# Kernel tuning notes

Measured on AMD Instinct MI355X. Metric: run time of the kernel, lower is better.

The kernel has to match this reference:

```python
import jax, jax.numpy as jnp
import numpy as np

K = 16          # buckets per codeblock (2**treeDepth)
DEPTH = 4       # tree depth
C = 256         # codeblockCount
IN_FEATURES = 4096
OUT_FEATURES = 4096
N_ROWS = 4096

_BASE_TREE = np.array([
    [-1,-1,0,-1,0,0,0,-1,0,0,0,0,0,0,0],[-1,-1,0,-1,0,0,0,1,0,0,0,0,0,0,0],
    [-1,-1,0,1,0,0,0,0,-1,0,0,0,0,0,0],[-1,-1,0,1,0,0,0,0,1,0,0,0,0,0,0],
    [-1,1,0,0,-1,0,0,0,0,-1,0,0,0,0,0],[-1,1,0,0,-1,0,0,0,0,1,0,0,0,0,0],
    [-1,1,0,0,1,0,0,0,0,0,-1,0,0,0,0],[-1,1,0,0,1,0,0,0,0,0,1,0,0,0,0],
    [1,0,-1,0,0,-1,0,0,0,0,0,-1,0,0,0],[1,0,-1,0,0,-1,0,0,0,0,0,1,0,0,0],
    [1,0,-1,0,0,1,0,0,0,0,0,0,-1,0,0],[1,0,-1,0,0,1,0,0,0,0,0,0,1,0,0],
    [1,0,1,0,0,0,-1,0,0,0,0,0,0,-1,0],[1,0,1,0,0,0,-1,0,0,0,0,0,0,1,0],
    [1,0,1,0,0,0,1,0,0,0,0,0,0,0,-1],[1,0,1,0,0,0,1,0,0,0,0,0,0,0,1]],
    dtype=np.float32)

def _make_tree_des_matrix(c):
    # NOTE: original code initializes with ONES, then overwrites diagonal blocks
    m = np.ones((c * K, c * (K - 1)), dtype=np.float32)
    for i in range(c):
        m[i*K:(i+1)*K, i*(K-1):(i+1)*(K-1)] = _BASE_TREE
    return m

def _make_selection_matrix(c):
    base = np.zeros((K - 1, DEPTH), dtype=np.float32)
    base[0, 0] = 1.0
    for i in range(1, K - 1):
        base[i, int(np.log2(i + 1))] = 1.0
    m = np.zeros((c * (K - 1), c * DEPTH), dtype=np.float32)
    for i in range(c):
        m[i*(K-1):(i+1)*(K-1), i*DEPTH:(i+1)*DEPTH] = base
    return m

def setup_inputs() -> dict:
    key = jax.random.key(0)
    k1, k2, k3, k4 = jax.random.split(key, 4)
    inputMatrix = jax.random.normal(k1, (N_ROWS, IN_FEATURES), dtype=jnp.float32)
    dims = jax.random.randint(k2, (C * DEPTH,), 0, IN_FEATURES)
    selection_matrix = jnp.asarray(_make_selection_matrix(C))
    thresholds = jax.random.normal(k3, (C * (K - 1), 1), dtype=jnp.float32)
    tree_des_mat = jnp.asarray(_make_tree_des_matrix(C))
    lut = jax.random.normal(k4, (OUT_FEATURES, C, K), dtype=jnp.float32)
    return {"inputMatrix": inputMatrix, "dims": dims,
            "selection_matrix": selection_matrix, "thresholds": thresholds,
            "tree_des_mat": tree_des_mat, "lut": lut}

def reference(inputMatrix, dims, selection_matrix, thresholds, tree_des_mat, lut):
    n = inputMatrix.shape[0]
    c = lut.shape[1]
    # gather the tree-split feature dims: (N, C*DEPTH)
    chosen = inputMatrix[:, dims]
    # (C*15, N)
    subtracted = selection_matrix @ chosen.T - thresholds
    tanh_h = jnp.tanh(subtracted)
    sign_ste = jnp.sign(subtracted) - jax.lax.stop_gradient(tanh_h) + tanh_h
    # (C*16, N) -> (N, C, 16)
    tree_result = (tree_des_mat @ sign_ste).T.reshape(n, c, K)
    encoding_soft = jax.nn.softmax(tree_result, axis=2)
    index = jnp.argmax(encoding_soft, axis=2)
    encoding_hard = jax.nn.one_hot(index, K, dtype=encoding_soft.dtype)
    Encoded = encoding_hard - jax.lax.stop_gradient(encoding_soft) + encoding_soft
    # LUT lookup: einsum 'nij,kij->nki' + sum over i, fused to 'nij,kij->nk'
    out = jnp.einsum('nij,kij->nk', Encoded, lut)
    return out
```

## Files before the change

### kernel.cpp

```cpp
#include <hip/hip_runtime.h>

#define N_ROWS 4096
#define IN_F   4096
#define OUT_F  4096
#define C_CB   256
#define KDIM   4096

typedef short bf16x8 __attribute__((ext_vector_type(8)));
typedef float f32x4  __attribute__((ext_vector_type(4)));

union ABFrag { unsigned long long u[2]; bf16x8 v; };

__device__ __forceinline__ unsigned int f2bf(float f) {
    unsigned int u = __builtin_bit_cast(unsigned int, f);
    return (u + 0x7FFFu + ((u >> 16) & 1u)) >> 16;
}

__global__ void k_idx(const float* __restrict__ input, const int* __restrict__ dims,
                      const float* __restrict__ thr, unsigned char* __restrict__ idx4) {
    const int n = blockIdx.x;
    const int c = threadIdx.x;
    const float* row = input + (size_t)n * IN_F;
    int4 d = *(const int4*)(dims + c * 4);
    const float* th = thr + c * 15;
    float x0 = row[d.x], x1 = row[d.y], x2 = row[d.z], x3 = row[d.w];
    int b0 = x0 > th[0];
    int j1 = 1 + b0;
    int b1 = x1 > th[j1];
    int j2 = 2 * j1 + 1 + b1;
    int b2 = x2 > th[j2];
    int j3 = 2 * j2 + 1 + b2;
    int b3 = x3 > th[j3];
    int idx = (b0 << 3) | (b1 << 2) | (b2 << 1) | b3;
    int other = __shfl_xor(idx, 1);
    if (!(c & 1))
        idx4[(c >> 1) * N_ROWS + n] = (unsigned char)(idx | (other << 4));
}

__global__ void k_cvt(const float* __restrict__ lut, unsigned short* __restrict__ lutb) {
    const int i = (blockIdx.x * blockDim.x + threadIdx.x) * 8;
    float4 a = *(const float4*)(lut + i);
    float4 b = *(const float4*)(lut + i + 4);
    uint4 o;
    o.x = f2bf(a.x) | (f2bf(a.y) << 16);
    o.y = f2bf(a.z) | (f2bf(a.w) << 16);
    o.z = f2bf(b.x) | (f2bf(b.y) << 16);
    o.w = f2bf(b.z) | (f2bf(b.w) << 16);
    *(uint4*)(lutb + i) = o;
}

#define BM 128
#define BN 128
#define BKT 64

template<bool STAGE_FP32>
__global__ __launch_bounds__(256, 4) void k_gemm(const unsigned short* __restrict__ lutb,
                                                 const float* __restrict__ lutf,
                                                 const unsigned char* __restrict__ idx4,
                                                 float* __restrict__ out) {
    __shared__ unsigned char smem[16384 + BN * BKT * 2];
    unsigned char* ish = smem;
    unsigned char* bsh = smem + 16384;

    const int t   = threadIdx.x;
    const int l15 = t & 15;
    const int q   = (t >> 4) & 3;
    const int w   = t >> 6;
    const int wm  = w >> 1, wn = w & 1;
    const int m0  = blockIdx.y * BM;
    const int n0  = blockIdx.x * BN;

    #pragma unroll
    for (int qq = 0; qq < 4; qq++) {
        int L = qq * 256 + t;
        const unsigned char* g = idx4 + (size_t)(L >> 3) * N_ROWS + m0 + (L & 7) * 16;
        __builtin_amdgcn_global_load_lds(
            (const __attribute__((address_space(1))) void*)g,
            (__attribute__((address_space(3))) void*)(ish + L * 16), 16, 0, 0);
    }

    f32x4 acc[4][4];
    #pragma unroll
    for (int mi = 0; mi < 4; mi++)
        #pragma unroll
        for (int ni = 0; ni < 4; ni++)
            acc[mi][ni] = (f32x4){0.f, 0.f, 0.f, 0.f};

    const int xorv = l15 & 7;
    const int bRowByte = (wn * 64 + l15) * (BKT * 2);
    const int aByte = wm * 64 + l15 * 4;
    const int qh4  = (q >> 1) * 4;
    const unsigned int sub8 = (q & 1) << 3;

    for (int kb = 0; kb < KDIM; kb += BKT) {
        if (!STAGE_FP32) {
            #pragma unroll
            for (int qq = 0; qq < 4; qq++) {
                int L = qq * 256 + t;
                int r = L >> 3, p = L & 7;
                int c = p ^ (r & 7);
                const unsigned short* g = lutb + (size_t)(n0 + r) * KDIM + kb + c * 8;
                __builtin_amdgcn_global_load_lds(
                    (const __attribute__((address_space(1))) void*)g,
                    (__attribute__((address_space(3))) void*)(bsh + L * 16), 16, 0, 0);
            }
        } else {
            #pragma unroll
            for (int qq = 0; qq < 4; qq++) {
                int L = qq * 256 + t;
                int r = L >> 3, p = L & 7;
                int c = p ^ (r & 7);
                const float* g = lutf + (size_t)(n0 + r) * KDIM + kb + c * 8;
                float4 f0 = *(const float4*)g;
                float4 f1 = *(const float4*)(g + 4);
                uint4 o;
                o.x = f2bf(f0.x) | (f2bf(f0.y) << 16);
                o.y = f2bf(f0.z) | (f2bf(f0.w) << 16);
                o.z = f2bf(f1.x) | (f2bf(f1.y) << 16);
                o.w = f2bf(f1.z) | (f2bf(f1.w) << 16);
                *(uint4*)(bsh + L * 16) = o;
            }
        }
        __syncthreads();

        #pragma unroll
        for (int s = 0; s < 2; s++) {
            const int cbp = (kb >> 5) + s;

            ABFrag bf[4];
            const int chunkOff = ((s * 4 + q) ^ xorv) * 16;
            #pragma unroll
            for (int ni = 0; ni < 4; ni++)
                bf[ni].v = *(const bf16x8*)(bsh + bRowByte + ni * (16 * BKT * 2) + chunkOff);

            const unsigned int w32 = *(const unsigned int*)(ish + cbp * 128 + aByte);

            ABFrag af[4];
            #pragma unroll
            for (int mi = 0; mi < 4; mi++) {
                unsigned int T = (w32 >> (mi * 8 + qh4)) & 0xFu;
                unsigned int rel = T - sub8;
                unsigned long long sh = 0x3F80ull << ((rel & 3) << 4);
                af[mi].u[0] = (rel < 4u) ? sh : 0ull;
                af[mi].u[1] = ((rel - 4u) < 4u) ? sh : 0ull;
            }

            #pragma unroll
            for (int mi = 0; mi < 4; mi++)
                #pragma unroll
                for (int ni = 0; ni < 4; ni++)
                    acc[mi][ni] = __builtin_amdgcn_mfma_f32_16x16x32_bf16(
                        af[mi].v, bf[ni].v, acc[mi][ni], 0, 0, 0);
        }
        __syncthreads();
    }

    #pragma unroll
    for (int mi = 0; mi < 4; mi++) {
        #pragma unroll
        for (int ni = 0; ni < 4; ni++) {
            const int col = n0 + wn * 64 + ni * 16 + l15;
            #pragma unroll
            for (int r = 0; r < 4; r++) {
                const int row = m0 + wm * 64 + 4 * (q * 4 + r) + mi;
                out[(size_t)row * OUT_F + col] = acc[mi][ni][r];
            }
        }
    }
}

extern "C" void kernel_launch(void* const* d_in, const int* in_sizes, int n_in,
                              void* d_out, int out_size, void* d_ws, size_t ws_size,
                              hipStream_t stream) {
    const float* input = (const float*)d_in[0];
    const int*   dims  = (const int*)d_in[1];
    const float* thr   = (const float*)d_in[3];
    const float* lut   = (const float*)d_in[5];
    float* out = (float*)d_out;

    const size_t lutbBytes = (size_t)OUT_F * KDIM * 2;
    const size_t idxBytes  = (size_t)(C_CB / 2) * N_ROWS;

    dim3 gg(OUT_F / BN, N_ROWS / BM);

    if (ws_size >= lutbBytes + idxBytes) {
        unsigned short* lutb = (unsigned short*)d_ws;
        unsigned char*  idx4 = (unsigned char*)d_ws + lutbBytes;
        k_idx<<<N_ROWS, C_CB, 0, stream>>>(input, dims, thr, idx4);
        k_cvt<<<(OUT_F * KDIM) / (256 * 8), 256, 0, stream>>>(lut, lutb);
        k_gemm<false><<<gg, 256, 0, stream>>>(lutb, lut, idx4, out);
    } else {
        unsigned char* idx4 = (unsigned char*)d_ws;
        k_idx<<<N_ROWS, C_CB, 0, stream>>>(input, dims, thr, idx4);
        k_gemm<true><<<gg, 256, 0, stream>>>(nullptr, lut, idx4, out);
    }
}
```

Baseline: 314.5 us.

## Load GEMM operands directly from global memory and fuse prep kernels

```diff
diff --git a/kernel.cpp b/kernel.cpp
--- a/kernel.cpp
+++ b/kernel.cpp
@@ -16,8 +16,42 @@
     return (u + 0x7FFFu + ((u >> 16) & 1u)) >> 16;
 }
 
-__global__ void k_idx(const float* __restrict__ input, const int* __restrict__ dims,
-                      const float* __restrict__ thr, unsigned char* __restrict__ idx4) {
+__global__ void k_prep(const float* __restrict__ input, const int* __restrict__ dims,
+                       const float* __restrict__ thr, unsigned char* __restrict__ idx4,
+                       const float* __restrict__ lut, unsigned short* __restrict__ lutb) {
+    if (blockIdx.x < N_ROWS) {
+        const int n = blockIdx.x;
+        const int c = threadIdx.x;
+        const float* row = input + (size_t)n * IN_F;
+        int4 d = *(const int4*)(dims + c * 4);
+        const float* th = thr + c * 15;
+        float x0 = row[d.x], x1 = row[d.y], x2 = row[d.z], x3 = row[d.w];
+        int b0 = x0 > th[0];
+        int j1 = 1 + b0;
+        int b1 = x1 > th[j1];
+        int j2 = 2 * j1 + 1 + b1;
+        int b2 = x2 > th[j2];
+        int j3 = 2 * j2 + 1 + b2;
+        int b3 = x3 > th[j3];
+        int idx = (b0 << 3) | (b1 << 2) | (b2 << 1) | b3;
+        int other = __shfl_xor(idx, 1);
+        if (!(c & 1))
+            idx4[(c >> 1) * N_ROWS + n] = (unsigned char)(idx | (other << 4));
+    } else {
+        const int i = ((blockIdx.x - N_ROWS) * 256 + threadIdx.x) * 8;
+        float4 a = *(const float4*)(lut + i);
+        float4 b = *(const float4*)(lut + i + 4);
+        uint4 o;
+        o.x = f2bf(a.x) | (f2bf(a.y) << 16);
+        o.y = f2bf(a.z) | (f2bf(a.w) << 16);
+        o.z = f2bf(b.x) | (f2bf(b.y) << 16);
+        o.w = f2bf(b.z) | (f2bf(b.w) << 16);
+        *(uint4*)(lutb + i) = o;
+    }
+}
+
+__global__ void k_idx_only(const float* __restrict__ input, const int* __restrict__ dims,
+                           const float* __restrict__ thr, unsigned char* __restrict__ idx4) {
     const int n = blockIdx.x;
     const int c = threadIdx.x;
     const float* row = input + (size_t)n * IN_F;
@@ -37,31 +71,14 @@
         idx4[(c >> 1) * N_ROWS + n] = (unsigned char)(idx | (other << 4));
 }
 
-__global__ void k_cvt(const float* __restrict__ lut, unsigned short* __restrict__ lutb) {
-    const int i = (blockIdx.x * blockDim.x + threadIdx.x) * 8;
-    float4 a = *(const float4*)(lut + i);
-    float4 b = *(const float4*)(lut + i + 4);
-    uint4 o;
-    o.x = f2bf(a.x) | (f2bf(a.y) << 16);
-    o.y = f2bf(a.z) | (f2bf(a.w) << 16);
-    o.z = f2bf(b.x) | (f2bf(b.y) << 16);
-    o.w = f2bf(b.z) | (f2bf(b.w) << 16);
-    *(uint4*)(lutb + i) = o;
-}
-
 #define BM 128
 #define BN 128
-#define BKT 64
 
-template<bool STAGE_FP32>
+template<bool B_IS_BF16>
 __global__ __launch_bounds__(256, 4) void k_gemm(const unsigned short* __restrict__ lutb,
                                                  const float* __restrict__ lutf,
                                                  const unsigned char* __restrict__ idx4,
                                                  float* __restrict__ out) {
-    __shared__ unsigned char smem[16384 + BN * BKT * 2];
-    unsigned char* ish = smem;
-    unsigned char* bsh = smem + 16384;
-
     const int t   = threadIdx.x;
     const int l15 = t & 15;
     const int q   = (t >> 4) & 3;
@@ -70,15 +87,6 @@
     const int m0  = blockIdx.y * BM;
     const int n0  = blockIdx.x * BN;
 
-    #pragma unroll
-    for (int qq = 0; qq < 4; qq++) {
-        int L = qq * 256 + t;
-        const unsigned char* g = idx4 + (size_t)(L >> 3) * N_ROWS + m0 + (L & 7) * 16;
-        __builtin_amdgcn_global_load_lds(
-            (const __attribute__((address_space(1))) void*)g,
-            (__attribute__((address_space(3))) void*)(ish + L * 16), 16, 0, 0);
-    }
-
     f32x4 acc[4][4];
     #pragma unroll
     for (int mi = 0; mi < 4; mi++)
@@ -86,73 +94,61 @@
         for (int ni = 0; ni < 4; ni++)
             acc[mi][ni] = (f32x4){0.f, 0.f, 0.f, 0.f};
 
-    const int xorv = l15 & 7;
-    const int bRowByte = (wn * 64 + l15) * (BKT * 2);
-    const int aByte = wm * 64 + l15 * 4;
-    const int qh4  = (q >> 1) * 4;
+    const int qh4 = (q >> 1) * 4;
     const unsigned int sub8 = (q & 1) << 3;
+    const size_t bRow = (size_t)(n0 + wn * 64 + l15) * KDIM;
+    const unsigned char* ibase = idx4 + m0 + wm * 64 + l15 * 4;
 
-    for (int kb = 0; kb < KDIM; kb += BKT) {
-        if (!STAGE_FP32) {
+    for (int kb = 0; kb < KDIM; kb += 64) {
+        ABFrag bf[2][4];
+        if (B_IS_BF16) {
             #pragma unroll
-            for (int qq = 0; qq < 4; qq++) {
-                int L = qq * 256 + t;
-                int r = L >> 3, p = L & 7;
-                int c = p ^ (r & 7);
-                const unsigned short* g = lutb + (size_t)(n0 + r) * KDIM + kb + c * 8;
-                __builtin_amdgcn_global_load_lds(
-                    (const __attribute__((address_space(1))) void*)g,
-                    (__attribute__((address_space(3))) void*)(bsh + L * 16), 16, 0, 0);
-            }
+            for (int s = 0; s < 2; s++)
+                #pragma unroll
+                for (int ni = 0; ni < 4; ni++)
+                    bf[s][ni].v = *(const bf16x8*)(lutb + bRow + (size_t)ni * 16 * KDIM
+                                                   + kb + s * 32 + q * 8);
         } else {
             #pragma unroll
-            for (int qq = 0; qq < 4; qq++) {
-                int L = qq * 256 + t;
-                int r = L >> 3, p = L & 7;
-                int c = p ^ (r & 7);
-                const float* g = lutf + (size_t)(n0 + r) * KDIM + kb + c * 8;
-                float4 f0 = *(const float4*)g;
-                float4 f1 = *(const float4*)(g + 4);
-                uint4 o;
-                o.x = f2bf(f0.x) | (f2bf(f0.y) << 16);
-                o.y = f2bf(f0.z) | (f2bf(f0.w) << 16);
-                o.z = f2bf(f1.x) | (f2bf(f1.y) << 16);
-                o.w = f2bf(f1.z) | (f2bf(f1.w) << 16);
-                *(uint4*)(bsh + L * 16) = o;
-            }
+            for (int s = 0; s < 2; s++)
+                #pragma unroll
+                for (int ni = 0; ni < 4; ni++) {
+                    const float* g = lutf + bRow + (size_t)ni * 16 * KDIM + kb + s * 32 + q * 8;
+                    float4 f0 = *(const float4*)g;
+                    float4 f1 = *(const float4*)(g + 4);
+                    uint4 o;
+                    o.x = f2bf(f0.x) | (f2bf(f0.y) << 16);
+                    o.y = f2bf(f0.z) | (f2bf(f0.w) << 16);
+                    o.z = f2bf(f1.x) | (f2bf(f1.y) << 16);
+                    o.w = f2bf(f1.z) | (f2bf(f1.w) << 16);
+                    bf[s][ni].u[0] = ((unsigned long long)o.y << 32) | o.x;
+                    bf[s][ni].u[1] = ((unsigned long long)o.w << 32) | o.z;
+                }
         }
-        __syncthreads();
+
+        unsigned int w32[2];
+        #pragma unroll
+        for (int s = 0; s < 2; s++)
+            w32[s] = *(const unsigned int*)(ibase + (size_t)((kb >> 5) + s) * N_ROWS);
 
         #pragma unroll
         for (int s = 0; s < 2; s++) {
-            const int cbp = (kb >> 5) + s;
-
-            ABFrag bf[4];
-            const int chunkOff = ((s * 4 + q) ^ xorv) * 16;
-            #pragma unroll
-            for (int ni = 0; ni < 4; ni++)
-                bf[ni].v = *(const bf16x8*)(bsh + bRowByte + ni * (16 * BKT * 2) + chunkOff);
-
-            const unsigned int w32 = *(const unsigned int*)(ish + cbp * 128 + aByte);
-
             ABFrag af[4];
             #pragma unroll
             for (int mi = 0; mi < 4; mi++) {
-                unsigned int T = (w32 >> (mi * 8 + qh4)) & 0xFu;
+                unsigned int T = (w32[s] >> (mi * 8 + qh4)) & 0xFu;
                 unsigned int rel = T - sub8;
                 unsigned long long sh = 0x3F80ull << ((rel & 3) << 4);
                 af[mi].u[0] = (rel < 4u) ? sh : 0ull;
                 af[mi].u[1] = ((rel - 4u) < 4u) ? sh : 0ull;
             }
-
             #pragma unroll
             for (int mi = 0; mi < 4; mi++)
                 #pragma unroll
                 for (int ni = 0; ni < 4; ni++)
                     acc[mi][ni] = __builtin_amdgcn_mfma_f32_16x16x32_bf16(
-                        af[mi].v, bf[ni].v, acc[mi][ni], 0, 0, 0);
+                        af[mi].v, bf[s][ni].v, acc[mi][ni], 0, 0, 0);
         }
-        __syncthreads();
     }
 
     #pragma unroll
@@ -186,12 +182,12 @@
     if (ws_size >= lutbBytes + idxBytes) {
         unsigned short* lutb = (unsigned short*)d_ws;
         unsigned char*  idx4 = (unsigned char*)d_ws + lutbBytes;
-        k_idx<<<N_ROWS, C_CB, 0, stream>>>(input, dims, thr, idx4);
-        k_cvt<<<(OUT_F * KDIM) / (256 * 8), 256, 0, stream>>>(lut, lutb);
-        k_gemm<false><<<gg, 256, 0, stream>>>(lutb, lut, idx4, out);
+        k_prep<<<N_ROWS + (OUT_F * KDIM) / (256 * 8), 256, 0, stream>>>(
+            input, dims, thr, idx4, lut, lutb);
+        k_gemm<true><<<gg, 256, 0, stream>>>(lutb, lut, idx4, out);
     } else {
         unsigned char* idx4 = (unsigned char*)d_ws;
-        k_idx<<<N_ROWS, C_CB, 0, stream>>>(input, dims, thr, idx4);
-        k_gemm<true><<<gg, 256, 0, stream>>>(nullptr, lut, idx4, out);
+        k_idx_only<<<N_ROWS, C_CB, 0, stream>>>(input, dims, thr, idx4);
+        k_gemm<false><<<gg, 256, 0, stream>>>(nullptr, lut, idx4, out);
     }
 }
```

Result: slower. 440.8 us (+40.1%).
